# Kernel optimization log

Measured on AMD Instinct MI355X. Metric: run time of the kernel, lower is better.

The kernel has to match this reference:

```python
import jax, jax.numpy as jnp
import numpy as np

IN_F, OUT_F, N_CLASSES, HEADS = 512, 64, 40, 4
B, M = 1, 4096
NEG_SLOPE = 0.01  # F.leaky_relu called with default slope (self.alpha unused)


def _xavier(key, shape, gain=1.0):
    fan_in, fan_out = shape[-1], shape[-2] if len(shape) > 1 else shape[-1]
    a = gain * np.sqrt(6.0 / (fan_in + fan_out))
    return jax.random.uniform(key, shape, jnp.float32, -a, a)


def setup_inputs() -> dict:
    key = jax.random.key(0)
    ks = jax.random.split(key, 12)
    h = jax.random.normal(ks[0], (B, M, IN_F), jnp.float32)
    A = jax.random.randint(ks[1], (B, M, M), 0, 2, jnp.int32)
    A = jnp.maximum(A, jnp.eye(M, dtype=jnp.int32)[None])  # self-loops avoid empty softmax rows
    return {
        "h": h,
        "A": A,
        "W1_w": _xavier(ks[2], (OUT_F * HEADS, IN_F)),
        "W1_b": jnp.zeros((OUT_F * HEADS,), jnp.float32),
        "a1": _xavier(ks[3], (HEADS, 2 * OUT_F), gain=1.414),
        "W3_w": _xavier(ks[4], (OUT_F, OUT_F * HEADS)),
        "W3_b": jnp.zeros((OUT_F,), jnp.float32),
        "W2_w": _xavier(ks[5], (OUT_F * HEADS, OUT_F)),
        "W2_b": jnp.zeros((OUT_F * HEADS,), jnp.float32),
        "a2": _xavier(ks[6], (HEADS, 2 * OUT_F)),
        "FL_w": _xavier(ks[7], (N_CLASSES, OUT_F * HEADS)),
        "FL_b": jnp.zeros((N_CLASSES,), jnp.float32),
    }


def _attention_block(h, mask, W_w, W_b, a):
    # h: (b,m,n); mask: (b,m,m) bool; W_w: (heads*out, n); a: (heads, 2*out)
    b, m, _ = h.shape
    Wh = jnp.einsum('bmn,on->bmo', h, W_w) + W_b          # (b,m,heads*out)
    Wh = Wh.reshape(b, m, HEADS, -1)                       # (b,m,h,c)
    c = Wh.shape[-1]
    src = jnp.einsum('bmhc,hc->bmh', Wh, a[:, :c])         # score from edge source i
    dst = jnp.einsum('bmhc,hc->bmh', Wh, a[:, c:])         # score from edge target j
    logits = jax.nn.leaky_relu(src[:, :, None, :] + dst[:, None, :, :], NEG_SLOPE)  # (b,i,j,h)
    logits = jnp.where(mask[..., None], logits, -jnp.inf)
    probs = jax.nn.softmax(logits, axis=2)                 # softmax over neighbors j
    out = jnp.einsum('bijh,bjhc->bihc', probs, Wh)
    return out.reshape(b, m, HEADS * c)


def reference(h, A, W1_w, W1_b, a1, W3_w, W3_b, W2_w, W2_b, a2, FL_w, FL_b):
    mask = A == 1
    x = _attention_block(h, mask, W1_w, W1_b, a1)          # (b,m,heads*out)
    x = jnp.einsum('bmo,po->bmp', x, W3_w) + W3_b          # (b,m,out)
    x = _attention_block(x, mask, W2_w, W2_b, a2)          # (b,m,heads*out)
    out = jnp.einsum('bmo,ko->bmk', x, FL_w) + FL_b        # (b,m,n_classes)
    return (x, out)
```

## Files before the change

### kernel.cpp

```cpp
#include <hip/hip_runtime.h>
#include <hip/hip_bf16.h>

typedef _Float16 f16_t;
typedef unsigned short u16;
typedef unsigned int u32;
typedef float f32x4 __attribute__((ext_vector_type(4)));
typedef f16_t f16x8 __attribute__((ext_vector_type(8)));
typedef u16 u16x8 __attribute__((ext_vector_type(8)));
typedef u16 u16x4 __attribute__((ext_vector_type(4)));
typedef u32 u32x4 __attribute__((ext_vector_type(4)));

#define MROWS 4096
#define NHEADS 4
#define COUT 64
#define OHF 256
#define NCLS 40
#define LOG2E 1.4426950408889634f
#define PLD 264

static __device__ __forceinline__ u16 f16b(float x) {
    return __builtin_bit_cast(u16, (f16_t)x);
}
static __device__ __forceinline__ float f16f(u16 x) {
    return (float)__builtin_bit_cast(f16_t, x);
}
static __device__ __forceinline__ float dmu_decode(u32 ku) {
    const u32 fb = (ku & 0x80000000u) ? (ku ^ 0x80000000u) : ~ku;
    return __builtin_bit_cast(float, fb);
}
static __device__ __forceinline__ float wave_sum(float v) {
    v += __shfl_xor(v, 1);  v += __shfl_xor(v, 2);  v += __shfl_xor(v, 4);
    v += __shfl_xor(v, 8);  v += __shfl_xor(v, 16); v += __shfl_xor(v, 32);
    return v;
}

__global__ __launch_bounds__(256) void prep_kernel(const float* __restrict__ W1w,
                                                   const float* __restrict__ W1b,
                                                   const float* __restrict__ a1,
                                                   const float* __restrict__ W2w,
                                                   const float* __restrict__ W2b,
                                                   const float* __restrict__ W3w,
                                                   const float* __restrict__ W3b,
                                                   const float* __restrict__ a2,
                                                   float* __restrict__ Cwf,
                                                   float* __restrict__ cbf,
                                                   float* __restrict__ va1,
                                                   float* __restrict__ vc1,
                                                   float* __restrict__ va2,
                                                   float* __restrict__ vc2,
                                                   u32* __restrict__ dmu) {
    __shared__ float u[8][64];
    const int bx = blockIdx.x, tid = threadIdx.x;
    const int lane = tid & 63, wv = tid >> 6;
    if (bx < 256) {
        float acc = 0.f;
        for (int t = 0; t < 64; ++t)
            acc += W2w[bx * 64 + t] * W3w[t * 256 + tid];
        Cwf[bx * 256 + tid] = acc;
        if (tid < 64) {
            float pb = W2w[bx * 64 + tid] * W3b[tid];
            pb = wave_sum(pb);
            if (tid == 0) cbf[bx] = pb + W2b[bx];
        }
    } else if (bx < 258) {
        const int k = (bx - 256) * 256 + tid;
#pragma unroll
        for (int hs = 0; hs < 8; ++hs) {
            const int h = hs >> 1, s = hs & 1;
            float acc = 0.f;
            for (int c = 0; c < COUT; ++c)
                acc += W1w[(size_t)(h * COUT + c) * 512 + k] * a1[h * 128 + s * COUT + c];
            va1[hs * 512 + k] = acc;
        }
        {
            const int hs = (bx - 256) * 4 + wv;
            const int h = hs >> 1, s = hs & 1;
            float pb = W1b[h * COUT + lane] * a1[h * 128 + s * COUT + lane];
            pb = wave_sum(pb);
            if (lane == 0) vc1[hs] = pb;
        }
    } else if (bx == 258) {
#pragma unroll
        for (int e = tid * 2; e < tid * 2 + 2; ++e) {
            const int hs = e >> 6, t = e & 63;
            const int h = hs >> 1, s = hs & 1;
            float acc = 0.f;
            for (int c = 0; c < COUT; ++c)
                acc += W2w[(size_t)(h * COUT + c) * 64 + t] * a2[h * 128 + s * COUT + c];
            u[hs][t] = acc;
        }
        __syncthreads();
#pragma unroll
        for (int hs = 0; hs < 8; ++hs) {
            float acc = 0.f;
            for (int t = 0; t < 64; ++t) acc += u[hs][t] * W3w[t * 256 + tid];
            va2[hs * 256 + tid] = acc;
        }
#pragma unroll
        for (int rep = 0; rep < 2; ++rep) {
            const int hs = wv + rep * 4;
            const int h = hs >> 1, s = hs & 1;
            float pb = u[hs][lane] * W3b[lane] +
                       W2b[h * COUT + lane] * a2[h * 128 + s * COUT + lane];
            pb = wave_sum(pb);
            if (lane == 0) vc2[hs] = pb;
        }
    } else {
        if (tid < 8) dmu[tid] = 0u;
    }
}

__global__ __launch_bounds__(256) void work_kernel(const float* __restrict__ X,
                                                   const float* __restrict__ Bm,
                                                   const float* __restrict__ bias,
                                                   int K,
                                                   u16* __restrict__ WhF,
                                                   const float* __restrict__ va,
                                                   const float* __restrict__ vc,
                                                   float* __restrict__ srcT,
                                                   float* __restrict__ dstT,
                                                   u32* __restrict__ dmu,
                                                   const int* __restrict__ A,
                                                   u32* __restrict__ AbitsT) {
    __shared__ __align__(16) unsigned char smem[19456];
    const int bx = blockIdx.x, tid = threadIdx.x;
    if (bx >= 512) {
        u32 (*nib)[1024] = (u32(*)[1024])smem;
        const int i0 = (bx - 512) * 2;
        u32 nb[8];
#pragma unroll
        for (int q = 0; q < 8; ++q) {
            const int r = q >> 2;
            const int col = (q & 3) * 1024 + tid * 4;
            const int4 v = *(const int4*)&A[(size_t)(i0 + r) * MROWS + col];
            nb[q] = (u32)(v.x != 0) | ((u32)(v.y != 0) << 1) |
                    ((u32)(v.z != 0) << 2) | ((u32)(v.w != 0) << 3);
        }
#pragma unroll
        for (int q = 0; q < 8; ++q)
            nib[q >> 2][(q & 3) * 256 + tid] = nb[q];
        __syncthreads();
        {
            const int r = tid >> 7, jw = tid & 127;
            const u32x4 n0 = *(const u32x4*)&nib[r][8 * jw];
            const u32x4 n1 = *(const u32x4*)&nib[r][8 * jw + 4];
            u32 word = n0[0] | (n0[1] << 4) | (n0[2] << 8) | (n0[3] << 12) |
                       (n1[0] << 16) | (n1[1] << 20) | (n1[2] << 24) | (n1[3] << 28);
            AbitsT[(size_t)jw * MROWS + i0 + r] = word;
        }
        return;
    }
    if (bx < 256) {
        u16 (*Al)[40] = (u16(*)[40])smem;
        u16 (*Bl)[40] = (u16(*)[40])(smem + 5120);
        u16 (*Tl)[72] = (u16(*)[72])(smem + 10240);
        const int lane = tid & 63, wv = tid >> 6;
        const int l15 = lane & 15, g = lane >> 4;
        const int m0 = (bx & 63) * 64, n0 = (bx >> 6) * 64;
        const int r = tid >> 2, c8 = (tid & 3) * 8;
        f32x4 acc[4] = {};
        for (int k0 = 0; k0 < K; k0 += 32) {
            const float4 a0 = *(const float4*)&X[(size_t)(m0 + r) * K + k0 + c8];
            const float4 a1 = *(const float4*)&X[(size_t)(m0 + r) * K + k0 + c8 + 4];
            const float4 b0 = *(const float4*)&Bm[(size_t)(n0 + r) * K + k0 + c8];
            const float4 b1 = *(const float4*)&Bm[(size_t)(n0 + r) * K + k0 + c8 + 4];
            u16x8 av, bv;
            av[0] = f16b(a0.x); av[1] = f16b(a0.y); av[2] = f16b(a0.z); av[3] = f16b(a0.w);
            av[4] = f16b(a1.x); av[5] = f16b(a1.y); av[6] = f16b(a1.z); av[7] = f16b(a1.w);
            bv[0] = f16b(b0.x); bv[1] = f16b(b0.y); bv[2] = f16b(b0.z); bv[3] = f16b(b0.w);
            bv[4] = f16b(b1.x); bv[5] = f16b(b1.y); bv[6] = f16b(b1.z); bv[7] = f16b(b1.w);
            __syncthreads();
            *(u16x8*)&Al[r][c8] = av;
            *(u16x8*)&Bl[r][c8] = bv;
            __syncthreads();
            f16x8 afr = *(const f16x8*)&Al[16 * wv + l15][8 * g];
#pragma unroll
            for (int ni = 0; ni < 4; ++ni) {
                f16x8 bfr = *(const f16x8*)&Bl[16 * ni + l15][8 * g];
                acc[ni] = __builtin_amdgcn_mfma_f32_16x16x32_f16(afr, bfr, acc[ni], 0, 0, 0);
            }
        }
#pragma unroll
        for (int ni = 0; ni < 4; ++ni) {
            const int nl = 16 * ni + l15;
            const float bvs = bias[n0 + nl];
#pragma unroll
            for (int rr = 0; rr < 4; ++rr)
                Tl[nl][16 * wv + 4 * g + rr] = f16b(acc[ni][rr] + bvs);
        }
        __syncthreads();
        const int jb0 = m0 >> 5;
#pragma unroll
        for (int q = 0; q < 2; ++q) {
            const int id = tid + 256 * q;
            const int jb_l = id >> 8, rem = id & 255;
            const int c_l = rem >> 2, gf = rem & 3;
            u16x8 v = *(const u16x8*)&Tl[c_l][32 * jb_l + 8 * gf];
            *(u16x8*)&WhF[(size_t)(((jb0 + jb_l) * 256 + n0 + c_l) * 4 + gf) * 8] = v;
        }
        return;
    }
    float (*red)[16][9] = (float(*)[16][9])smem;
    float (*dred)[16]   = (float(*)[16])(smem + 9216);
    const int bs = bx - 256;
    const int ii = tid >> 4, ki = tid & 15;
    const int i = bs * 16 + ii;
    const int KS = K >> 4;
    const int k0 = ki * KS;
    float acc[8] = {};
    for (int k = k0; k < k0 + KS; k += 4) {
        const float4 xv = *(const float4*)&X[(size_t)i * K + k];
#pragma unroll
        for (int hs = 0; hs < 8; ++hs) {
            const float4 vv = *(const float4*)&va[(size_t)hs * K + k];
            acc[hs] += xv.x * vv.x + xv.y * vv.y + xv.z * vv.z + xv.w * vv.w;
        }
    }
#pragma unroll
    for (int hs = 0; hs < 8; ++hs) red[ii][ki][hs] = acc[hs];
    __syncthreads();
    if (tid < 128) {
        const int row = tid >> 3, hs = tid & 7, h = hs >> 1;
        float sum = 0.f;
#pragma unroll
        for (int kk = 0; kk < 16; ++kk) sum += red[row][kk][hs];
        const float val = sum + vc[hs];
        const int ig = bs * 16 + row;
        if ((hs & 1) == 0) {
            srcT[h * MROWS + ig] = val;
        } else {
            dstT[h * MROWS + ig] = val;
            dred[h][row] = val;
        }
    }
    __syncthreads();
    if (tid < 4) {
        float m = -3.4e38f;
#pragma unroll
        for (int r = 0; r < 16; ++r) m = fmaxf(m, dred[tid][r]);
        const u32 b = __builtin_bit_cast(u32, m);
        const u32 key = (b & 0x80000000u) ? ~b : (b | 0x80000000u);
        atomicMax(dmu + tid, key);
    }
}

template <int JT>
__global__ __launch_bounds__(512, 4) void attn_kernel(const u16* __restrict__ WhF,
                                                      const float* __restrict__ srcT,
                                                      const float* __restrict__ dstT,
                                                      const u32* __restrict__ AbitsT,
                                                      const u32* __restrict__ dmu,
                                                      u16* __restrict__ partial,
                                                      float* __restrict__ outF) {
    constexpr int J64 = JT * 64;
    constexpr int NSTEP = 2 * JT;
    __shared__ __align__(16) float GT[8 * J64];
    const int tid = threadIdx.x;
    const int lane = tid & 63, w = tid >> 6;
    const int h = w & 3, mi = w >> 2;
    const int l15 = lane & 15, g = lane >> 4;
    const int i0 = blockIdx.x * 32;
    const int chunk = blockIdx.y;
    const int jbase = chunk * J64;

    for (int e = tid; e < 8 * J64; e += 512) {
        const int hb = e / J64;
        const int j = e - hb * J64;
        const float dmhe = dmu_decode(dmu[hb >> 1]);
        const float sc = (hb & 1) ? 0.01f * LOG2E : LOG2E;
        GT[e] = __builtin_amdgcn_exp2f((dstT[(hb >> 1) * MROWS + jbase + j] - dmhe) * sc);
    }

    const float dmh = dmu_decode(dmu[h]);
    const float s = srcT[h * MROWS + i0 + 16 * mi + l15];
    const float sd = s + dmh;
    const float C = fmaxf(sd, 0.01f * sd);
    const float F1 = __builtin_amdgcn_exp2f((sd - C) * LOG2E);
    const float F2 = __builtin_amdgcn_exp2f((0.01f * sd - C) * LOG2E);
    __syncthreads();

    f32x4 acc[4] = {};
    f32x4 acc1 = {};
    f16x8 ones;
#pragma unroll
    for (int e = 0; e < 8; ++e) ones[e] = (f16_t)1.0f;
    const int irow = i0 + 16 * mi + l15;
    const int jb0 = jbase >> 5;
    const int cb = h * COUT + l15;

    u32 curW = AbitsT[(size_t)jb0 * MROWS + irow];
    f16x8 cB0 = *(const f16x8*)&WhF[(size_t)((((jb0) << 8) + cb) * 4 + g) * 8];
    f16x8 cB1 = *(const f16x8*)&WhF[(size_t)((((jb0) << 8) + cb + 16) * 4 + g) * 8];
    f16x8 cB2 = *(const f16x8*)&WhF[(size_t)((((jb0) << 8) + cb + 32) * 4 + g) * 8];
    f16x8 cB3 = *(const f16x8*)&WhF[(size_t)((((jb0) << 8) + cb + 48) * 4 + g) * 8];

#pragma unroll
    for (int t = 0; t < NSTEP; ++t) {
        u32 nW = 0;
        f16x8 nB0 = {}, nB1 = {}, nB2 = {}, nB3 = {};
        if (t + 1 < NSTEP) {
            const int jb = jb0 + t + 1;
            nW = AbitsT[(size_t)jb * MROWS + irow];
            nB0 = *(const f16x8*)&WhF[(size_t)(((jb << 8) + cb) * 4 + g) * 8];
            nB1 = *(const f16x8*)&WhF[(size_t)(((jb << 8) + cb + 16) * 4 + g) * 8];
            nB2 = *(const f16x8*)&WhF[(size_t)(((jb << 8) + cb + 32) * 4 + g) * 8];
            nB3 = *(const f16x8*)&WhF[(size_t)(((jb << 8) + cb + 48) * 4 + g) * 8];
        }
        const int goff = t * 32 + 8 * g;
        const float4 g10 = *(const float4*)&GT[(h * 2) * J64 + goff];
        const float4 g11 = *(const float4*)&GT[(h * 2) * J64 + goff + 4];
        const float4 g20 = *(const float4*)&GT[(h * 2 + 1) * J64 + goff];
        const float4 g21 = *(const float4*)&GT[(h * 2 + 1) * J64 + goff + 4];
        const float G1[8] = {g10.x, g10.y, g10.z, g10.w, g11.x, g11.y, g11.z, g11.w};
        const float G2[8] = {g20.x, g20.y, g20.z, g20.w, g21.x, g21.y, g21.z, g21.w};
        const u32 bits = (curW >> (8 * g)) & 0xffu;
        f16x8 a;
#pragma unroll
        for (int e = 0; e < 8; ++e) {
            float wv = fmaxf(G1[e] * F1, G2[e] * F2);
            wv = ((bits >> e) & 1u) ? wv : 0.f;
            a[e] = (f16_t)wv;
        }
        __builtin_amdgcn_s_setprio(1);
        acc[0] = __builtin_amdgcn_mfma_f32_16x16x32_f16(a, cB0, acc[0], 0, 0, 0);
        acc[1] = __builtin_amdgcn_mfma_f32_16x16x32_f16(a, cB1, acc[1], 0, 0, 0);
        acc[2] = __builtin_amdgcn_mfma_f32_16x16x32_f16(a, cB2, acc[2], 0, 0, 0);
        acc[3] = __builtin_amdgcn_mfma_f32_16x16x32_f16(a, cB3, acc[3], 0, 0, 0);
        acc1 = __builtin_amdgcn_mfma_f32_16x16x32_f16(a, ones, acc1, 0, 0, 0);
        __builtin_amdgcn_s_setprio(0);
        curW = nW;
        cB0 = nB0; cB1 = nB1; cB2 = nB2; cB3 = nB3;
    }

    if (partial) {
        u16* pc = partial + (size_t)chunk * MROWS * PLD;
#pragma unroll
        for (int ni = 0; ni < 4; ++ni)
#pragma unroll
            for (int rr = 0; rr < 4; ++rr) {
                const int i = i0 + 16 * mi + 4 * g + rr;
                pc[(size_t)i * PLD + h * COUT + 16 * ni + l15] = f16b(acc[ni][rr]);
            }
#pragma unroll
        for (int rr = 0; rr < 4; ++rr)
            if (l15 == rr)
                pc[(size_t)(i0 + 16 * mi + 4 * g + rr) * PLD + 256 + h] = f16b(acc1[rr]);
    } else {
#pragma unroll
        for (int rr = 0; rr < 4; ++rr) {
            const int i = i0 + 16 * mi + 4 * g + rr;
            const float rs = acc1[rr];
#pragma unroll
            for (int ni = 0; ni < 4; ++ni)
                outF[(size_t)i * OHF + h * COUT + 16 * ni + l15] = acc[ni][rr] / rs;
        }
    }
}

__global__ __launch_bounds__(256) void combine_kernel(const u16* __restrict__ partial,
                                                      int nchunk,
                                                      float* __restrict__ outF,
                                                      const float* __restrict__ FLw,
                                                      const float* __restrict__ FLb,
                                                      float* __restrict__ outL) {
    __shared__ float xrow[256];
    __shared__ float cred[40][4];
    const int i = blockIdx.x, c = threadIdx.x, h = c >> 6;
    float v = 0.f, rs = 0.f;
    for (int ch = 0; ch < nchunk; ++ch) {
        const u16* pc = partial + (size_t)ch * MROWS * PLD + (size_t)i * PLD;
        v += f16f(pc[c]);
        rs += f16f(pc[256 + h]);
    }
    const float r = v / rs;
    outF[(size_t)i * OHF + c] = r;
    if (!FLw) return;
    xrow[c] = r;
    __syncthreads();
    if (c < 160) {
        const int k = c >> 2, seg = c & 3;
        const float* xp = &xrow[seg * 64];
        const float* wp = &FLw[(size_t)k * OHF + seg * 64];
        float a = 0.f;
#pragma unroll
        for (int t = 0; t < 64; t += 4) {
            const float4 x4 = *(const float4*)&xp[t];
            const float4 w4 = *(const float4*)&wp[t];
            a += x4.x * w4.x + x4.y * w4.y + x4.z * w4.z + x4.w * w4.w;
        }
        cred[k][seg] = a;
    }
    __syncthreads();
    if (c < NCLS)
        outL[(size_t)i * NCLS + c] = cred[c][0] + cred[c][1] + cred[c][2] + cred[c][3] + FLb[c];
}

extern "C" void kernel_launch(void* const* d_in, const int* in_sizes, int n_in,
                              void* d_out, int out_size, void* d_ws, size_t ws_size,
                              hipStream_t stream) {
    const float* hIn = (const float*)d_in[0];
    const int*   A   = (const int*)d_in[1];
    const float* W1w = (const float*)d_in[2];
    const float* W1b = (const float*)d_in[3];
    const float* a1  = (const float*)d_in[4];
    const float* W3w = (const float*)d_in[5];
    const float* W3b = (const float*)d_in[6];
    const float* W2w = (const float*)d_in[7];
    const float* W2b = (const float*)d_in[8];
    const float* a2  = (const float*)d_in[9];
    const float* FLw = (const float*)d_in[10];
    const float* FLb = (const float*)d_in[11];
    float* outX = (float*)d_out;
    float* outL = outX + (size_t)MROWS * OHF;

    char* p = (char*)d_ws;
    auto alloc = [&](size_t bytes) { char* q = p; p += (bytes + 255) & ~(size_t)255; return q; };
    u32*   AbitsT = (u32*)alloc((size_t)MROWS * 128 * 4);
    u16*   WhF1  = (u16*)alloc((size_t)OHF * MROWS * 2);
    u16*   WhF2  = (u16*)alloc((size_t)OHF * MROWS * 2);
    float* x1f   = (float*)alloc((size_t)MROWS * OHF * 4);
    float* Cwf   = (float*)alloc((size_t)256 * 256 * 4);
    float* cbf   = (float*)alloc(256 * 4);
    float* va1   = (float*)alloc((size_t)8 * 512 * 4);
    float* vc1   = (float*)alloc(8 * 4);
    float* va2   = (float*)alloc((size_t)8 * 256 * 4);
    float* vc2   = (float*)alloc(8 * 4);
    float* srcT1 = (float*)alloc((size_t)NHEADS * MROWS * 4);
    float* dstT1 = (float*)alloc((size_t)NHEADS * MROWS * 4);
    float* srcT2 = (float*)alloc((size_t)NHEADS * MROWS * 4);
    float* dstT2 = (float*)alloc((size_t)NHEADS * MROWS * 4);
    u32*   dmu   = (u32*)alloc(8 * 4);
    size_t fixed = (size_t)(p - (char*)d_ws);
    int nchunk = 8;
    if (fixed + (size_t)8 * MROWS * PLD * 2 > ws_size) nchunk = 4;
    u16* partial = (u16*)p;

    dim3 blk(256);
    prep_kernel<<<dim3(260), blk, 0, stream>>>(W1w, W1b, a1, W2w, W2b, W3w, W3b, a2,
                                               Cwf, cbf, va1, vc1, va2, vc2, dmu);

    auto launch_attn = [&](const u16* WhF, const float* srcT, const float* dstT,
                           const u32* dm) {
        if (nchunk == 8)
            attn_kernel<8><<<dim3(128, 8), dim3(512), 0, stream>>>(WhF, srcT, dstT, AbitsT, dm, partial, nullptr);
        else
            attn_kernel<16><<<dim3(128, 4), dim3(512), 0, stream>>>(WhF, srcT, dstT, AbitsT, dm, partial, nullptr);
    };

    work_kernel<<<dim3(2560), blk, 0, stream>>>(hIn, W1w, W1b, 512, WhF1,
                                                va1, vc1, srcT1, dstT1, dmu,
                                                A, AbitsT);
    launch_attn(WhF1, srcT1, dstT1, dmu);
    combine_kernel<<<dim3(4096), blk, 0, stream>>>(partial, nchunk, x1f,
                                                   nullptr, nullptr, nullptr);

    work_kernel<<<dim3(512), blk, 0, stream>>>(x1f, Cwf, cbf, 256, WhF2,
                                               va2, vc2, srcT2, dstT2, dmu + 4,
                                               A, AbitsT);
    launch_attn(WhF2, srcT2, dstT2, dmu + 4);
    combine_kernel<<<dim3(4096), blk, 0, stream>>>(partial, nchunk, outX,
                                                   FLw, FLb, outL);
}
```

Baseline: 167.1 us.

## Read adjacency mask directly in attention instead of precomputing packed bit transpose

Removes the adjacency bit-packing pass from the first projection kernel and has each attention kernel read the int32 adjacency rows directly, testing each element as the mask. The chunk count is also fixed at four with the larger JT=16 tile. This drops a separate packing phase and its workspace buffer, but each attention pass now streams the full 64MB int32 matrix instead of a 2MB bitmap, doubling total adjacency traffic.

```diff
diff --git a/kernel.cpp b/kernel.cpp
--- a/kernel.cpp
+++ b/kernel.cpp
@@ -8,7 +8,6 @@
 typedef f16_t f16x8 __attribute__((ext_vector_type(8)));
 typedef u16 u16x8 __attribute__((ext_vector_type(8)));
 typedef u16 u16x4 __attribute__((ext_vector_type(4)));
-typedef u32 u32x4 __attribute__((ext_vector_type(4)));
 
 #define MROWS 4096
 #define NHEADS 4
@@ -119,37 +118,9 @@
                                                    const float* __restrict__ vc,
                                                    float* __restrict__ srcT,
                                                    float* __restrict__ dstT,
-                                                   u32* __restrict__ dmu,
-                                                   const int* __restrict__ A,
-                                                   u32* __restrict__ AbitsT) {
+                                                   u32* __restrict__ dmu) {
     __shared__ __align__(16) unsigned char smem[19456];
     const int bx = blockIdx.x, tid = threadIdx.x;
-    if (bx >= 512) {
-        u32 (*nib)[1024] = (u32(*)[1024])smem;
-        const int i0 = (bx - 512) * 2;
-        u32 nb[8];
-#pragma unroll
-        for (int q = 0; q < 8; ++q) {
-            const int r = q >> 2;
-            const int col = (q & 3) * 1024 + tid * 4;
-            const int4 v = *(const int4*)&A[(size_t)(i0 + r) * MROWS + col];
-            nb[q] = (u32)(v.x != 0) | ((u32)(v.y != 0) << 1) |
-                    ((u32)(v.z != 0) << 2) | ((u32)(v.w != 0) << 3);
-        }
-#pragma unroll
-        for (int q = 0; q < 8; ++q)
-            nib[q >> 2][(q & 3) * 256 + tid] = nb[q];
-        __syncthreads();
-        {
-            const int r = tid >> 7, jw = tid & 127;
-            const u32x4 n0 = *(const u32x4*)&nib[r][8 * jw];
-            const u32x4 n1 = *(const u32x4*)&nib[r][8 * jw + 4];
-            u32 word = n0[0] | (n0[1] << 4) | (n0[2] << 8) | (n0[3] << 12) |
-                       (n1[0] << 16) | (n1[1] << 20) | (n1[2] << 24) | (n1[3] << 28);
-            AbitsT[(size_t)jw * MROWS + i0 + r] = word;
-        }
-        return;
-    }
     if (bx < 256) {
         u16 (*Al)[40] = (u16(*)[40])smem;
         u16 (*Bl)[40] = (u16(*)[40])(smem + 5120);
@@ -248,7 +219,7 @@
 __global__ __launch_bounds__(512, 4) void attn_kernel(const u16* __restrict__ WhF,
                                                       const float* __restrict__ srcT,
                                                       const float* __restrict__ dstT,
-                                                      const u32* __restrict__ AbitsT,
+                                                      const int* __restrict__ A,
                                                       const u32* __restrict__ dmu,
                                                       u16* __restrict__ partial,
                                                       float* __restrict__ outF) {
@@ -287,8 +258,10 @@
     const int irow = i0 + 16 * mi + l15;
     const int jb0 = jbase >> 5;
     const int cb = h * COUT + l15;
-
-    u32 curW = AbitsT[(size_t)jb0 * MROWS + irow];
+    const int* Arow = A + (size_t)irow * MROWS + 8 * g;
+
+    int4 cA0 = *(const int4*)&Arow[jb0 << 5];
+    int4 cA1 = *(const int4*)&Arow[(jb0 << 5) + 4];
     f16x8 cB0 = *(const f16x8*)&WhF[(size_t)((((jb0) << 8) + cb) * 4 + g) * 8];
     f16x8 cB1 = *(const f16x8*)&WhF[(size_t)((((jb0) << 8) + cb + 16) * 4 + g) * 8];
     f16x8 cB2 = *(const f16x8*)&WhF[(size_t)((((jb0) << 8) + cb + 32) * 4 + g) * 8];
@@ -296,11 +269,12 @@
 
 #pragma unroll
     for (int t = 0; t < NSTEP; ++t) {
-        u32 nW = 0;
+        int4 nA0 = {}, nA1 = {};
         f16x8 nB0 = {}, nB1 = {}, nB2 = {}, nB3 = {};
         if (t + 1 < NSTEP) {
             const int jb = jb0 + t + 1;
-            nW = AbitsT[(size_t)jb * MROWS + irow];
+            nA0 = *(const int4*)&Arow[jb << 5];
+            nA1 = *(const int4*)&Arow[(jb << 5) + 4];
             nB0 = *(const f16x8*)&WhF[(size_t)(((jb << 8) + cb) * 4 + g) * 8];
             nB1 = *(const f16x8*)&WhF[(size_t)(((jb << 8) + cb + 16) * 4 + g) * 8];
             nB2 = *(const f16x8*)&WhF[(size_t)(((jb << 8) + cb + 32) * 4 + g) * 8];
@@ -313,12 +287,12 @@
         const float4 g21 = *(const float4*)&GT[(h * 2 + 1) * J64 + goff + 4];
         const float G1[8] = {g10.x, g10.y, g10.z, g10.w, g11.x, g11.y, g11.z, g11.w};
         const float G2[8] = {g20.x, g20.y, g20.z, g20.w, g21.x, g21.y, g21.z, g21.w};
-        const u32 bits = (curW >> (8 * g)) & 0xffu;
+        const int msk[8] = {cA0.x, cA0.y, cA0.z, cA0.w, cA1.x, cA1.y, cA1.z, cA1.w};
         f16x8 a;
 #pragma unroll
         for (int e = 0; e < 8; ++e) {
             float wv = fmaxf(G1[e] * F1, G2[e] * F2);
-            wv = ((bits >> e) & 1u) ? wv : 0.f;
+            wv = msk[e] ? wv : 0.f;
             a[e] = (f16_t)wv;
         }
         __builtin_amdgcn_s_setprio(1);
@@ -328,7 +302,7 @@
         acc[3] = __builtin_amdgcn_mfma_f32_16x16x32_f16(a, cB3, acc[3], 0, 0, 0);
         acc1 = __builtin_amdgcn_mfma_f32_16x16x32_f16(a, ones, acc1, 0, 0, 0);
         __builtin_amdgcn_s_setprio(0);
-        curW = nW;
+        cA0 = nA0; cA1 = nA1;
         cB0 = nB0; cB1 = nB1; cB2 = nB2; cB3 = nB3;
     }
 
@@ -415,7 +389,6 @@
 
     char* p = (char*)d_ws;
     auto alloc = [&](size_t bytes) { char* q = p; p += (bytes + 255) & ~(size_t)255; return q; };
-    u32*   AbitsT = (u32*)alloc((size_t)MROWS * 128 * 4);
     u16*   WhF1  = (u16*)alloc((size_t)OHF * MROWS * 2);
     u16*   WhF2  = (u16*)alloc((size_t)OHF * MROWS * 2);
     float* x1f   = (float*)alloc((size_t)MROWS * OHF * 4);
@@ -430,34 +403,24 @@
     float* srcT2 = (float*)alloc((size_t)NHEADS * MROWS * 4);
     float* dstT2 = (float*)alloc((size_t)NHEADS * MROWS * 4);
     u32*   dmu   = (u32*)alloc(8 * 4);
-    size_t fixed = (size_t)(p - (char*)d_ws);
-    int nchunk = 8;
-    if (fixed + (size_t)8 * MROWS * PLD * 2 > ws_size) nchunk = 4;
+    const int nchunk = 4;
     u16* partial = (u16*)p;
 
     dim3 blk(256);
     prep_kernel<<<dim3(260), blk, 0, stream>>>(W1w, W1b, a1, W2w, W2b, W3w, W3b, a2,
                                                Cwf, cbf, va1, vc1, va2, vc2, dmu);
 
-    auto launch_attn = [&](const u16* WhF, const float* srcT, const float* dstT,
-                           const u32* dm) {
-        if (nchunk == 8)
-            attn_kernel<8><<<dim3(128, 8), dim3(512), 0, stream>>>(WhF, srcT, dstT, AbitsT, dm, partial, nullptr);
-        else
-            attn_kernel<16><<<dim3(128, 4), dim3(512), 0, stream>>>(WhF, srcT, dstT, AbitsT, dm, partial, nullptr);
-    };
-
-    work_kernel<<<dim3(2560), blk, 0, stream>>>(hIn, W1w, W1b, 512, WhF1,
-                                                va1, vc1, srcT1, dstT1, dmu,
-                                                A, AbitsT);
-    launch_attn(WhF1, srcT1, dstT1, dmu);
+    work_kernel<<<dim3(512), blk, 0, stream>>>(hIn, W1w, W1b, 512, WhF1,
+                                               va1, vc1, srcT1, dstT1, dmu);
+    attn_kernel<16><<<dim3(128, nchunk), dim3(512), 0, stream>>>(
+        WhF1, srcT1, dstT1, A, dmu, partial, nullptr);
     combine_kernel<<<dim3(4096), blk, 0, stream>>>(partial, nchunk, x1f,
                                                    nullptr, nullptr, nullptr);
 
     work_kernel<<<dim3(512), blk, 0, stream>>>(x1f, Cwf, cbf, 256, WhF2,
-                                               va2, vc2, srcT2, dstT2, dmu + 4,
-                                               A, AbitsT);
-    launch_attn(WhF2, srcT2, dstT2, dmu + 4);
+                                               va2, vc2, srcT2, dstT2, dmu + 4);
+    attn_kernel<16><<<dim3(128, nchunk), dim3(512), 0, stream>>>(
+        WhF2, srcT2, dstT2, A, dmu + 4, partial, nullptr);
     combine_kernel<<<dim3(4096), blk, 0, stream>>>(partial, nchunk, outX,
                                                    FLw, FLb, outL);
 }
```

After: 206.6 us. +23.7%, slower.
